# Kernel optimization log

Hardware: AMD Instinct MI355X
Metric: run time of the kernel (lower is better)

The kernel has to match this reference:

```python
import jax, jax.numpy as jnp
import numpy as np

WINDOW_SIZE = 11
SIGMA = 1.5
CHANNELS = 3
DATA_RANGE = 1.0


def _create_window(window_size, channel):
    x = np.arange(window_size) - window_size // 2
    g = np.exp(-(x ** 2) / (2.0 * SIGMA ** 2))
    g = g / g.sum()
    w2d = np.outer(g, g).astype(np.float32)  # [ws, ws]
    # depthwise kernel, OIHW with I=1, O=channel
    return jnp.asarray(np.broadcast_to(w2d, (channel, 1, window_size, window_size)).copy())


def _depthwise_conv(x, window, channel):
    # x: [B, C, H, W], window: [C, 1, ws, ws], VALID padding, groups=C
    return jax.lax.conv_general_dilated(
        x, window, window_strides=(1, 1), padding='VALID',
        dimension_numbers=('NCHW', 'OIHW', 'NCHW'),
        feature_group_count=channel)


def setup_inputs() -> dict:
    key = jax.random.key(0)
    k1, k2 = jax.random.split(key)
    img1 = jax.random.uniform(k1, (32, CHANNELS, 512, 512), dtype=jnp.float32)
    img2 = jax.random.uniform(k2, (32, CHANNELS, 512, 512), dtype=jnp.float32)
    return {"img1": img1, "img2": img2}


def reference(img1, img2):
    channel = img1.shape[1]
    window = _create_window(WINDOW_SIZE, channel).astype(img1.dtype)

    mu1 = _depthwise_conv(img1, window, channel)
    mu2 = _depthwise_conv(img2, window, channel)
    mu1_sq = mu1 * mu1
    mu2_sq = mu2 * mu2
    mu1_mu2 = mu1 * mu2

    sigma1_sq = _depthwise_conv(img1 * img1, window, channel) - mu1_sq
    sigma2_sq = _depthwise_conv(img2 * img2, window, channel) - mu2_sq
    sigma12 = _depthwise_conv(img1 * img2, window, channel) - mu1_mu2

    C1 = (0.01 * DATA_RANGE) ** 2
    C2 = (0.03 * DATA_RANGE) ** 2
    v1 = 2.0 * sigma12 + C2
    v2 = sigma1_sq + sigma2_sq + C2
    ssim_map = (2.0 * mu1_mu2 + C1) * v1 / ((mu1_sq + mu2_sq + C1) * v2)
    # mean over channel, height, width -> per-image SSIM [B]
    return ssim_map.mean(axis=(1, 2, 3))
```

## Files before the change

kernel.cpp:

```cpp
#include <hip/hip_runtime.h>
#include <math.h>

#define H 512
#define W 512
#define OUT_H 502
#define OUT_W 502
#define C1c 1.0e-4f
#define C2c 9.0e-4f

#define TH 56
#define NR (TH + 10)
#define RING_N 528

__global__ __launch_bounds__(256, 2)
void ssim_kernel(const float* __restrict__ img1,
                 const float* __restrict__ img2,
                 float* __restrict__ out) {
    __shared__ float2 ring[2][RING_N];
    __shared__ float wsum[4];

    const int tid = threadIdx.x;

    float g[11];
    {
        float s = 0.f;
#pragma unroll
        for (int i = 0; i < 11; ++i) {
            float d = (float)(i - 5);
            g[i] = expf(-d * d * (1.0f / 4.5f));
            s += g[i];
        }
        float inv = 1.0f / s;
#pragma unroll
        for (int i = 0; i < 11; ++i) {
            g[i] *= inv;
            g[i] = __uint_as_float(__builtin_amdgcn_readfirstlane(__float_as_uint(g[i])));
        }
    }

    const int oyb = blockIdx.x * TH;
    const int Y0  = min(oyb, H - NR);
    const int plane = blockIdx.y;
    const size_t pbase = (size_t)plane * (H * W);
    const float* __restrict__ p1 = img1 + pbase;
    const float* __restrict__ p2 = img2 + pbase;

    const int c0 = 2 * tid;
    const bool v0ok = (c0 < OUT_W);
    const bool v1ok = (c0 + 1 < OUT_W);

    if (tid < RING_N - W) {
        ring[0][W + tid] = make_float2(0.f, 0.f);
        ring[1][W + tid] = make_float2(0.f, 0.f);
    }

    float a0A[11], a1A[11], a2A[11], a3A[11], a4A[11];
    float a0B[11], a1B[11], a2B[11], a3B[11], a4B[11];
#pragma unroll
    for (int i = 0; i < 11; ++i) {
        a0A[i]=0.f; a1A[i]=0.f; a2A[i]=0.f; a3A[i]=0.f; a4A[i]=0.f;
        a0B[i]=0.f; a1B[i]=0.f; a2B[i]=0.f; a3B[i]=0.f; a4B[i]=0.f;
    }

    float lsum = 0.f;

    int fidx = Y0 * W + c0;
    const int fcap = (H - 1) * W + c0;
    float2 va = *(const float2*)(p1 + fidx);
    float2 vb = *(const float2*)(p2 + fidx);

#pragma unroll 1
    for (int rb = 0; rb < NR; rb += 11) {
#pragma unroll
        for (int p = 0; p < 11; ++p) {
            const int r = rb + p;
            const int slot = r & 1;

            *(float4*)&ring[slot][c0] = make_float4(va.x, vb.x, va.y, vb.y);

            fidx = min(fidx + W, fcap);
            va = *(const float2*)(p1 + fidx);
            vb = *(const float2*)(p2 + fidx);

            __syncthreads();

            float hA0=0.f,hA1=0.f,hA2=0.f,hA3=0.f,hA4=0.f;
            float hB0=0.f,hB1=0.f,hB2=0.f,hB3=0.f,hB4=0.f;
            const float4* rp = (const float4*)&ring[slot][c0];
#pragma unroll
            for (int k = 0; k < 6; ++k) {
                const float4 f = rp[k];
                {
                    const int e = 2 * k;
                    const float x = f.x, y = f.y;
                    const float q2 = x * x, q3 = y * y, q4 = x * y;
                    if (e <= 10) {
                        const float w = g[e];
                        hA0 = fmaf(w, x,  hA0); hA1 = fmaf(w, y,  hA1);
                        hA2 = fmaf(w, q2, hA2); hA3 = fmaf(w, q3, hA3);
                        hA4 = fmaf(w, q4, hA4);
                    }
                    if (e >= 1) {
                        const float w = g[e - 1];
                        hB0 = fmaf(w, x,  hB0); hB1 = fmaf(w, y,  hB1);
                        hB2 = fmaf(w, q2, hB2); hB3 = fmaf(w, q3, hB3);
                        hB4 = fmaf(w, q4, hB4);
                    }
                }
                {
                    const int e = 2 * k + 1;
                    const float x = f.z, y = f.w;
                    const float q2 = x * x, q3 = y * y, q4 = x * y;
                    if (e <= 10) {
                        const float w = g[e];
                        hA0 = fmaf(w, x,  hA0); hA1 = fmaf(w, y,  hA1);
                        hA2 = fmaf(w, q2, hA2); hA3 = fmaf(w, q3, hA3);
                        hA4 = fmaf(w, q4, hA4);
                    }
                    {
                        const float w = g[e - 1];
                        hB0 = fmaf(w, x,  hB0); hB1 = fmaf(w, y,  hB1);
                        hB2 = fmaf(w, q2, hB2); hB3 = fmaf(w, q3, hB3);
                        hB4 = fmaf(w, q4, hB4);
                    }
                }
            }

#pragma unroll
            for (int a = 0; a < 11; ++a) {
                const float w = g[(p - a + 11) % 11];
                a0A[a] = fmaf(w, hA0, a0A[a]); a1A[a] = fmaf(w, hA1, a1A[a]);
                a2A[a] = fmaf(w, hA2, a2A[a]); a3A[a] = fmaf(w, hA3, a3A[a]);
                a4A[a] = fmaf(w, hA4, a4A[a]);
                a0B[a] = fmaf(w, hB0, a0B[a]); a1B[a] = fmaf(w, hB1, a1B[a]);
                a2B[a] = fmaf(w, hB2, a2B[a]); a3B[a] = fmaf(w, hB3, a3B[a]);
                a4B[a] = fmaf(w, hB4, a4B[a]);
            }

            const int e = (p + 1) % 11;
            if (r >= 10) {
                const int oy = Y0 + r - 10;
                if (oy >= oyb) {
                    {
                        const float m1 = a0A[e], m2 = a1A[e];
                        const float m1s = m1 * m1, m2s = m2 * m2, m12 = m1 * m2;
                        const float sig1  = a2A[e] - m1s;
                        const float sig2  = a3A[e] - m2s;
                        const float sig12 = a4A[e] - m12;
                        const float num = (2.f * m12 + C1c) * (2.f * sig12 + C2c);
                        const float den = (m1s + m2s + C1c) * (sig1 + sig2 + C2c);
                        const float v = num * __builtin_amdgcn_rcpf(den);
                        if (v0ok) lsum += v;
                    }
                    {
                        const float m1 = a0B[e], m2 = a1B[e];
                        const float m1s = m1 * m1, m2s = m2 * m2, m12 = m1 * m2;
                        const float sig1  = a2B[e] - m1s;
                        const float sig2  = a3B[e] - m2s;
                        const float sig12 = a4B[e] - m12;
                        const float num = (2.f * m12 + C1c) * (2.f * sig12 + C2c);
                        const float den = (m1s + m2s + C1c) * (sig1 + sig2 + C2c);
                        const float v = num * __builtin_amdgcn_rcpf(den);
                        if (v1ok) lsum += v;
                    }
                }
            }
            a0A[e]=0.f; a1A[e]=0.f; a2A[e]=0.f; a3A[e]=0.f; a4A[e]=0.f;
            a0B[e]=0.f; a1B[e]=0.f; a2B[e]=0.f; a3B[e]=0.f; a4B[e]=0.f;
        }
    }

#pragma unroll
    for (int off = 32; off > 0; off >>= 1) lsum += __shfl_down(lsum, off, 64);
    if ((tid & 63) == 0) wsum[tid >> 6] = lsum;
    __syncthreads();
    if (tid == 0) {
        const float inv_count = 1.0f / (3.0f * (float)OUT_H * (float)OUT_W);
        const float total = (wsum[0] + wsum[1] + wsum[2] + wsum[3]) * inv_count;
        atomicAdd(&out[plane / 3], total);
    }
}

__global__ void zero_out(float* out, int n) {
    int i = threadIdx.x + blockIdx.x * blockDim.x;
    if (i < n) out[i] = 0.f;
}

extern "C" void kernel_launch(void* const* d_in, const int* in_sizes, int n_in,
                              void* d_out, int out_size, void* d_ws, size_t ws_size,
                              hipStream_t stream) {
    const float* img1 = (const float*)d_in[0];
    const float* img2 = (const float*)d_in[1];
    float* out = (float*)d_out;

    zero_out<<<1, 64, 0, stream>>>(out, out_size);

    const int nplanes = in_sizes[0] / (H * W);
    dim3 grid((OUT_H + TH - 1) / TH,
              nplanes);
    ssim_kernel<<<grid, 256, 0, stream>>>(img1, img2, out);
}
```

Before: 261.5 us.

## Use per-wave LDS staging with halo loads to replace block-wide barriers

Each wavefront now stages its own 128-column span plus a 10-column halo, loaded redundantly by five lanes, into a private LDS slot. This lets the per-row __syncthreads be replaced by wave barriers, removing the block-wide synchronisation on every input row. It also initialises accumulators by multiply instead of zeroing them plus an FMA, and replaces the output predicates with mask multiplies. The cost is extra halo global loads and a single-buffered per-wave staging area whose safety relies on wave-level ordering.

```diff
diff --git a/kernel.cpp b/kernel.cpp
--- a/kernel.cpp
+++ b/kernel.cpp
@@ -9,17 +9,20 @@
 #define C2c 9.0e-4f
 
 #define TH 56
-#define NR (TH + 10)
-#define RING_N 528
+#define NR 66
+#define WSPAN 128
+#define SLOTQ 72
 
 __global__ __launch_bounds__(256, 2)
 void ssim_kernel(const float* __restrict__ img1,
                  const float* __restrict__ img2,
                  float* __restrict__ out) {
-    __shared__ float2 ring[2][RING_N];
+    __shared__ float4 stg[4][SLOTQ];
     __shared__ float wsum[4];
 
-    const int tid = threadIdx.x;
+    const int tid  = threadIdx.x;
+    const int wid  = tid >> 6;
+    const int lane = tid & 63;
 
     float g[11];
     {
@@ -45,14 +48,13 @@
     const float* __restrict__ p1 = img1 + pbase;
     const float* __restrict__ p2 = img2 + pbase;
 
-    const int c0 = 2 * tid;
-    const bool v0ok = (c0 < OUT_W);
-    const bool v1ok = (c0 + 1 < OUT_W);
-
-    if (tid < RING_N - W) {
-        ring[0][W + tid] = make_float2(0.f, 0.f);
-        ring[1][W + tid] = make_float2(0.f, 0.f);
-    }
+    const int c0 = wid * WSPAN + 2 * lane;
+    const int ch = min(wid * WSPAN + 128 + 2 * lane, W - 2);
+    const bool hl = (lane < 5);
+    const float mA = (c0     < OUT_W) ? 1.0f : 0.0f;
+    const float mB = (c0 + 1 < OUT_W) ? 1.0f : 0.0f;
+
+    float4* const st = stg[wid];
 
     float a0A[11], a1A[11], a2A[11], a3A[11], a4A[11];
     float a0B[11], a1B[11], a2B[11], a3B[11], a4B[11];
@@ -64,81 +66,104 @@
 
     float lsum = 0.f;
 
-    int fidx = Y0 * W + c0;
-    const int fcap = (H - 1) * W + c0;
-    float2 va = *(const float2*)(p1 + fidx);
-    float2 vb = *(const float2*)(p2 + fidx);
+    int ro = Y0 * W;
+    const int rocap = (H - 1) * W;
+
+    float2 va = *(const float2*)(p1 + ro + c0);
+    float2 vb = *(const float2*)(p2 + ro + c0);
+    float2 ha = make_float2(0.f, 0.f), hb = make_float2(0.f, 0.f);
+    if (hl) { ha = *(const float2*)(p1 + ro + ch); hb = *(const float2*)(p2 + ro + ch); }
 
 #pragma unroll 1
     for (int rb = 0; rb < NR; rb += 11) {
 #pragma unroll
         for (int p = 0; p < 11; ++p) {
             const int r = rb + p;
-            const int slot = r & 1;
-
-            *(float4*)&ring[slot][c0] = make_float4(va.x, vb.x, va.y, vb.y);
-
-            fidx = min(fidx + W, fcap);
-            va = *(const float2*)(p1 + fidx);
-            vb = *(const float2*)(p2 + fidx);
-
-            __syncthreads();
-
-            float hA0=0.f,hA1=0.f,hA2=0.f,hA3=0.f,hA4=0.f;
-            float hB0=0.f,hB1=0.f,hB2=0.f,hB3=0.f,hB4=0.f;
-            const float4* rp = (const float4*)&ring[slot][c0];
-#pragma unroll
-            for (int k = 0; k < 6; ++k) {
-                const float4 f = rp[k];
-                {
-                    const int e = 2 * k;
-                    const float x = f.x, y = f.y;
-                    const float q2 = x * x, q3 = y * y, q4 = x * y;
-                    if (e <= 10) {
-                        const float w = g[e];
-                        hA0 = fmaf(w, x,  hA0); hA1 = fmaf(w, y,  hA1);
-                        hA2 = fmaf(w, q2, hA2); hA3 = fmaf(w, q3, hA3);
-                        hA4 = fmaf(w, q4, hA4);
-                    }
-                    if (e >= 1) {
-                        const float w = g[e - 1];
-                        hB0 = fmaf(w, x,  hB0); hB1 = fmaf(w, y,  hB1);
-                        hB2 = fmaf(w, q2, hB2); hB3 = fmaf(w, q3, hB3);
-                        hB4 = fmaf(w, q4, hB4);
-                    }
-                }
-                {
-                    const int e = 2 * k + 1;
-                    const float x = f.z, y = f.w;
-                    const float q2 = x * x, q3 = y * y, q4 = x * y;
-                    if (e <= 10) {
-                        const float w = g[e];
-                        hA0 = fmaf(w, x,  hA0); hA1 = fmaf(w, y,  hA1);
-                        hA2 = fmaf(w, q2, hA2); hA3 = fmaf(w, q3, hA3);
-                        hA4 = fmaf(w, q4, hA4);
-                    }
-                    {
-                        const float w = g[e - 1];
-                        hB0 = fmaf(w, x,  hB0); hB1 = fmaf(w, y,  hB1);
-                        hB2 = fmaf(w, q2, hB2); hB3 = fmaf(w, q3, hB3);
-                        hB4 = fmaf(w, q4, hB4);
+
+            st[lane] = make_float4(va.x, vb.x, va.y, vb.y);
+            if (hl) st[64 + lane] = make_float4(ha.x, hb.x, ha.y, hb.y);
+
+            ro = min(ro + W, rocap);
+            va = *(const float2*)(p1 + ro + c0);
+            vb = *(const float2*)(p2 + ro + c0);
+            if (hl) { ha = *(const float2*)(p1 + ro + ch); hb = *(const float2*)(p2 + ro + ch); }
+
+            __builtin_amdgcn_wave_barrier();
+
+            float hA0, hA1, hA2, hA3, hA4;
+            float hB0, hB1, hB2, hB3, hB4;
+            {
+                const float4* rp = st + lane;
+#pragma unroll
+                for (int k = 0; k < 6; ++k) {
+                    const float4 f = rp[k];
+                    {
+                        const int e = 2 * k;
+                        const float x1 = f.x, x2 = f.y;
+                        const float q11 = x1 * x1, q22 = x2 * x2, q12 = x1 * x2;
+                        if (e == 0) {
+                            const float w = g[0];
+                            hA0 = w * x1; hA1 = w * x2; hA2 = w * q11;
+                            hA3 = w * q22; hA4 = w * q12;
+                        } else if (e <= 10) {
+                            const float w = g[e];
+                            hA0 = fmaf(w, x1,  hA0); hA1 = fmaf(w, x2,  hA1);
+                            hA2 = fmaf(w, q11, hA2); hA3 = fmaf(w, q22, hA3);
+                            hA4 = fmaf(w, q12, hA4);
+                        }
+                        if (e >= 1) {
+                            const float w = g[e - 1];
+                            hB0 = fmaf(w, x1,  hB0); hB1 = fmaf(w, x2,  hB1);
+                            hB2 = fmaf(w, q11, hB2); hB3 = fmaf(w, q22, hB3);
+                            hB4 = fmaf(w, q12, hB4);
+                        }
+                    }
+                    {
+                        const int e = 2 * k + 1;
+                        const float x1 = f.z, x2 = f.w;
+                        const float q11 = x1 * x1, q22 = x2 * x2, q12 = x1 * x2;
+                        if (e <= 10) {
+                            const float w = g[e];
+                            hA0 = fmaf(w, x1,  hA0); hA1 = fmaf(w, x2,  hA1);
+                            hA2 = fmaf(w, q11, hA2); hA3 = fmaf(w, q22, hA3);
+                            hA4 = fmaf(w, q12, hA4);
+                        }
+                        if (e == 1) {
+                            const float w = g[0];
+                            hB0 = w * x1; hB1 = w * x2; hB2 = w * q11;
+                            hB3 = w * q22; hB4 = w * q12;
+                        } else {
+                            const float w = g[e - 1];
+                            hB0 = fmaf(w, x1,  hB0); hB1 = fmaf(w, x2,  hB1);
+                            hB2 = fmaf(w, q11, hB2); hB3 = fmaf(w, q22, hB3);
+                            hB4 = fmaf(w, q12, hB4);
+                        }
                     }
                 }
             }
 
+            __builtin_amdgcn_wave_barrier();
+
 #pragma unroll
             for (int a = 0; a < 11; ++a) {
                 const float w = g[(p - a + 11) % 11];
-                a0A[a] = fmaf(w, hA0, a0A[a]); a1A[a] = fmaf(w, hA1, a1A[a]);
-                a2A[a] = fmaf(w, hA2, a2A[a]); a3A[a] = fmaf(w, hA3, a3A[a]);
-                a4A[a] = fmaf(w, hA4, a4A[a]);
-                a0B[a] = fmaf(w, hB0, a0B[a]); a1B[a] = fmaf(w, hB1, a1B[a]);
-                a2B[a] = fmaf(w, hB2, a2B[a]); a3B[a] = fmaf(w, hB3, a3B[a]);
-                a4B[a] = fmaf(w, hB4, a4B[a]);
+                if (a == p) {
+                    a0A[a] = w * hA0; a1A[a] = w * hA1; a2A[a] = w * hA2;
+                    a3A[a] = w * hA3; a4A[a] = w * hA4;
+                    a0B[a] = w * hB0; a1B[a] = w * hB1; a2B[a] = w * hB2;
+                    a3B[a] = w * hB3; a4B[a] = w * hB4;
+                } else {
+                    a0A[a] = fmaf(w, hA0, a0A[a]); a1A[a] = fmaf(w, hA1, a1A[a]);
+                    a2A[a] = fmaf(w, hA2, a2A[a]); a3A[a] = fmaf(w, hA3, a3A[a]);
+                    a4A[a] = fmaf(w, hA4, a4A[a]);
+                    a0B[a] = fmaf(w, hB0, a0B[a]); a1B[a] = fmaf(w, hB1, a1B[a]);
+                    a2B[a] = fmaf(w, hB2, a2B[a]); a3B[a] = fmaf(w, hB3, a3B[a]);
+                    a4B[a] = fmaf(w, hB4, a4B[a]);
+                }
             }
 
-            const int e = (p + 1) % 11;
             if (r >= 10) {
+                const int e = (p + 1) % 11;
                 const int oy = Y0 + r - 10;
                 if (oy >= oyb) {
                     {
@@ -149,8 +174,7 @@
                         const float sig12 = a4A[e] - m12;
                         const float num = (2.f * m12 + C1c) * (2.f * sig12 + C2c);
                         const float den = (m1s + m2s + C1c) * (sig1 + sig2 + C2c);
-                        const float v = num * __builtin_amdgcn_rcpf(den);
-                        if (v0ok) lsum += v;
+                        lsum = fmaf(mA, num * __builtin_amdgcn_rcpf(den), lsum);
                     }
                     {
                         const float m1 = a0B[e], m2 = a1B[e];
@@ -160,19 +184,16 @@
                         const float sig12 = a4B[e] - m12;
                         const float num = (2.f * m12 + C1c) * (2.f * sig12 + C2c);
                         const float den = (m1s + m2s + C1c) * (sig1 + sig2 + C2c);
-                        const float v = num * __builtin_amdgcn_rcpf(den);
-                        if (v1ok) lsum += v;
+                        lsum = fmaf(mB, num * __builtin_amdgcn_rcpf(den), lsum);
                     }
                 }
             }
-            a0A[e]=0.f; a1A[e]=0.f; a2A[e]=0.f; a3A[e]=0.f; a4A[e]=0.f;
-            a0B[e]=0.f; a1B[e]=0.f; a2B[e]=0.f; a3B[e]=0.f; a4B[e]=0.f;
         }
     }
 
 #pragma unroll
     for (int off = 32; off > 0; off >>= 1) lsum += __shfl_down(lsum, off, 64);
-    if ((tid & 63) == 0) wsum[tid >> 6] = lsum;
+    if (lane == 0) wsum[wid] = lsum;
     __syncthreads();
     if (tid == 0) {
         const float inv_count = 1.0f / (3.0f * (float)OUT_H * (float)OUT_W);
```

Result: slower. 268.3 us (+2.6%).
